# Optimization experiments

Measured on AMD Instinct MI355X. Metric: run time of the kernel, lower is better.

The kernel has to match this reference:

```python
import jax, jax.numpy as jnp
import numpy as np

B, D = 500000, 3
EPS = 1e-8

def _matrix_sqrt_H(A):
    # Hermitian sqrt via eigh: Q diag((L^2)^0.25) Q^T  (matches torch code incl. |L| handling)
    L, Q = jnp.linalg.eigh(A)
    return jnp.einsum('bij,bj,bkj->bik', Q, (L ** 2) ** 0.25, Q)

def setup_inputs() -> dict:
    key = jax.random.key(0)
    k1, k2, k3, k4 = jax.random.split(key, 4)
    miu_1 = jax.random.normal(k1, (B, D), dtype=jnp.float32)
    miu_2 = jax.random.normal(k2, (B, D), dtype=jnp.float32)
    eye = jnp.eye(D, dtype=jnp.float32)
    M1 = jax.random.normal(k3, (B, D, D), dtype=jnp.float32)
    M2 = jax.random.normal(k4, (B, D, D), dtype=jnp.float32)
    # SPD covariances, as produced by a Gaussian-splatting pipeline
    cov_1 = 0.1 * jnp.einsum('bij,bkj->bik', M1, M1) + 1e-3 * eye
    cov_2 = 0.1 * jnp.einsum('bij,bkj->bik', M2, M2) + 1e-3 * eye
    return {"miu_1": miu_1, "miu_2": miu_2, "cov_1": cov_1, "cov_2": cov_2}

def reference(miu_1, miu_2, cov_1, cov_2):
    eye = jnp.eye(cov_1.shape[-1], dtype=cov_1.dtype)
    A_sqrt = _matrix_sqrt_H(cov_1 + eye * EPS)
    A_sqrt_inv = jnp.linalg.inv(A_sqrt + eye * EPS)
    C = jnp.einsum('bij,bjk,blk->bil', A_sqrt, cov_2, A_sqrt)  # A_sqrt cov_2 A_sqrt^T
    C_sqrt = _matrix_sqrt_H(C + eye * EPS)
    cov_velocity = jnp.einsum('bij,bjk,blk->bil', A_sqrt, C_sqrt, A_sqrt_inv)
    cov_velocity = cov_velocity + jnp.swapaxes(cov_velocity, -1, -2) - 2.0 * cov_1
    return (miu_2 - miu_1, cov_velocity)
```

## Files before the change

kernel.cpp:

```cpp
#include <hip/hip_runtime.h>
#include <math.h>

#define EPS 1e-8f

typedef float f4a __attribute__((ext_vector_type(4), aligned(4)));
typedef float f2a __attribute__((ext_vector_type(2), aligned(4)));

static __device__ __forceinline__ void jangle(float app, float aqq, float apq,
                                              float &c, float &s, float &app2, float &aqq2) {
    float h     = aqq - app;
    float ah    = fabsf(h) + 1e-18f;
    float v     = apq + apq;
    float rad   = fmaf(ah, ah, v * v);
    float rr    = __builtin_amdgcn_rsqf(rad);
    float c2h   = fmaf(0.5f * ah, rr, 0.5f);
    float rc2   = __builtin_amdgcn_rsqf(c2h);
    c = c2h * rc2;
    float apq_s = (h < 0.0f) ? -apq : apq;
    s = apq_s * (rr * rc2);
    float dl    = copysignf(0.5f * (rad * rr - ah), h);
    app2 = app - dl;
    aqq2 = aqq + dl;
}

static __device__ __forceinline__ void eigh3(
    float &a00, float &a01, float &a02, float &a11, float &a12, float &a22,
    float &q00, float &q01, float &q02,
    float &q10, float &q11, float &q12,
    float &q20, float &q21, float &q22)
{
    float c, s, x, y, t0, t1;
    jangle(a00, a11, a01, c, s, x, y); a00 = x; a11 = y; a01 = 0.0f;
    t0 = a02; t1 = a12; a02 = fmaf(c, t0, -s * t1); a12 = fmaf(c, t1, s * t0);
    q00 = c; q01 = s; q10 = -s; q11 = c;

    jangle(a00, a22, a02, c, s, x, y); a00 = x; a22 = y; a02 = 0.0f;
    t0 = a01; t1 = a12; a01 = fmaf(c, t0, -s * t1); a12 = fmaf(c, t1, s * t0);
    q02 = s * q00; q12 = s * q10; q20 = -s; q22 = c;
    q00 = c * q00; q10 = c * q10;

    jangle(a11, a22, a12, c, s, x, y); a11 = x; a22 = y; a12 = 0.0f;
    t0 = a01; t1 = a02; a01 = fmaf(c, t0, -s * t1); a02 = fmaf(c, t1, s * t0);
    t0 = q01; t1 = q02; q01 = fmaf(c, t0, -s * t1); q02 = fmaf(s, t0, c * t1);
    t0 = q11; t1 = q12; q11 = fmaf(c, t0, -s * t1); q12 = fmaf(s, t0, c * t1);
    q21 = -s * q22; q22 = c * q22;

    #pragma unroll
    for (int sw = 0; sw < 2; ++sw) {
        jangle(a00, a11, a01, c, s, x, y); a00 = x; a11 = y; a01 = 0.0f;
        t0 = a02; t1 = a12; a02 = fmaf(c, t0, -s * t1); a12 = fmaf(c, t1, s * t0);
        t0 = q00; t1 = q01; q00 = fmaf(c, t0, -s * t1); q01 = fmaf(s, t0, c * t1);
        t0 = q10; t1 = q11; q10 = fmaf(c, t0, -s * t1); q11 = fmaf(s, t0, c * t1);
        t0 = q20; t1 = q21; q20 = fmaf(c, t0, -s * t1); q21 = fmaf(s, t0, c * t1);

        jangle(a00, a22, a02, c, s, x, y); a00 = x; a22 = y; a02 = 0.0f;
        t0 = a01; t1 = a12; a01 = fmaf(c, t0, -s * t1); a12 = fmaf(c, t1, s * t0);
        t0 = q00; t1 = q02; q00 = fmaf(c, t0, -s * t1); q02 = fmaf(s, t0, c * t1);
        t0 = q10; t1 = q12; q10 = fmaf(c, t0, -s * t1); q12 = fmaf(s, t0, c * t1);
        t0 = q20; t1 = q22; q20 = fmaf(c, t0, -s * t1); q22 = fmaf(s, t0, c * t1);

        jangle(a11, a22, a12, c, s, x, y); a11 = x; a22 = y; a12 = 0.0f;
        t0 = a01; t1 = a02; a01 = fmaf(c, t0, -s * t1); a02 = fmaf(c, t1, s * t0);
        t0 = q01; t1 = q02; q01 = fmaf(c, t0, -s * t1); q02 = fmaf(s, t0, c * t1);
        t0 = q11; t1 = q12; q11 = fmaf(c, t0, -s * t1); q12 = fmaf(s, t0, c * t1);
        t0 = q21; t1 = q22; q21 = fmaf(c, t0, -s * t1); q22 = fmaf(s, t0, c * t1);
    }
}

static __device__ __forceinline__ void wlog_elem(
    float k00, float k01, float k02, float k11, float k12, float k22,
    float m00, float m01, float m02, float m11, float m12, float m22,
    float &o00, float &o01, float &o02, float &o11, float &o12, float &o22)
{
    float a00 = k00 + EPS, a01 = k01, a02 = k02,
          a11 = k11 + EPS, a12 = k12, a22 = k22 + EPS;
    float q00, q01, q02, q10, q11, q12, q20, q21, q22;
    eigh3(a00, a01, a02, a11, a12, a22,
          q00, q01, q02, q10, q11, q12, q20, q21, q22);

    float w0 = fmaxf(fabsf(a00), 1e-12f);
    float w1 = fmaxf(fabsf(a11), 1e-12f);
    float w2 = fmaxf(fabsf(a22), 1e-12f);
    float di0 = __builtin_amdgcn_rsqf(w0), di1 = __builtin_amdgcn_rsqf(w1),
          di2 = __builtin_amdgcn_rsqf(w2);
    float d0 = w0 * di0, d1 = w1 * di1, d2 = w2 * di2;

    float T00 = fmaf(m00, q00, fmaf(m01, q10, m02 * q20));
    float T01 = fmaf(m00, q01, fmaf(m01, q11, m02 * q21));
    float T02 = fmaf(m00, q02, fmaf(m01, q12, m02 * q22));
    float T10 = fmaf(m01, q00, fmaf(m11, q10, m12 * q20));
    float T11 = fmaf(m01, q01, fmaf(m11, q11, m12 * q21));
    float T12 = fmaf(m01, q02, fmaf(m11, q12, m12 * q22));
    float T20 = fmaf(m02, q00, fmaf(m12, q10, m22 * q20));
    float T21 = fmaf(m02, q01, fmaf(m12, q11, m22 * q21));
    float T22 = fmaf(m02, q02, fmaf(m12, q12, m22 * q22));

    float g00 = fmaf(q00, T00, fmaf(q10, T10, q20 * T20));
    float g01 = fmaf(q00, T01, fmaf(q10, T11, q20 * T21));
    float g02 = fmaf(q00, T02, fmaf(q10, T12, q20 * T22));
    float g11 = fmaf(q01, T01, fmaf(q11, T11, q21 * T21));
    float g12 = fmaf(q01, T02, fmaf(q11, T12, q21 * T22));
    float g22 = fmaf(q02, T02, fmaf(q12, T12, q22 * T22));

    float cp00 = fmaf(w0, g00, EPS);
    float cp11 = fmaf(w1, g11, EPS);
    float cp22 = fmaf(w2, g22, EPS);
    float cp01 = d0 * d1 * g01;
    float cp02 = d0 * d2 * g02;
    float cp12 = d1 * d2 * g12;

    float e00, e01, e02, e10, e11, e12, e20, e21, e22;
    eigh3(cp00, cp01, cp02, cp11, cp12, cp22,
          e00, e01, e02, e10, e11, e12, e20, e21, e22);
    float u0 = fmaxf(fabsf(cp00), 1e-12f);
    float u1 = fmaxf(fabsf(cp11), 1e-12f);
    float u2 = fmaxf(fabsf(cp22), 1e-12f);
    float ts0 = u0 * __builtin_amdgcn_rsqf(u0);
    float ts1 = u1 * __builtin_amdgcn_rsqf(u1);
    float ts2 = u2 * __builtin_amdgcn_rsqf(u2);

    float Ed00 = d0*e00, Ed01 = d0*e01, Ed02 = d0*e02;
    float Ed10 = d1*e10, Ed11 = d1*e11, Ed12 = d1*e12;
    float Ed20 = d2*e20, Ed21 = d2*e21, Ed22 = d2*e22;
    float Ei00 = di0*e00, Ei01 = di0*e01, Ei02 = di0*e02;
    float Ei10 = di1*e10, Ei11 = di1*e11, Ei12 = di1*e12;
    float Ei20 = di2*e20, Ei21 = di2*e21, Ei22 = di2*e22;

    float U00 = fmaf(q00, Ed00, fmaf(q01, Ed10, q02 * Ed20));
    float U01 = fmaf(q00, Ed01, fmaf(q01, Ed11, q02 * Ed21));
    float U02 = fmaf(q00, Ed02, fmaf(q01, Ed12, q02 * Ed22));
    float U10 = fmaf(q10, Ed00, fmaf(q11, Ed10, q12 * Ed20));
    float U11 = fmaf(q10, Ed01, fmaf(q11, Ed11, q12 * Ed21));
    float U12 = fmaf(q10, Ed02, fmaf(q11, Ed12, q12 * Ed22));
    float U20 = fmaf(q20, Ed00, fmaf(q21, Ed10, q22 * Ed20));
    float U21 = fmaf(q20, Ed01, fmaf(q21, Ed11, q22 * Ed21));
    float U22 = fmaf(q20, Ed02, fmaf(q21, Ed12, q22 * Ed22));

    float P00 = fmaf(q00, Ei00, fmaf(q01, Ei10, q02 * Ei20));
    float P01 = fmaf(q00, Ei01, fmaf(q01, Ei11, q02 * Ei21));
    float P02 = fmaf(q00, Ei02, fmaf(q01, Ei12, q02 * Ei22));
    float P10 = fmaf(q10, Ei00, fmaf(q11, Ei10, q12 * Ei20));
    float P11 = fmaf(q10, Ei01, fmaf(q11, Ei11, q12 * Ei21));
    float P12 = fmaf(q10, Ei02, fmaf(q11, Ei12, q12 * Ei22));
    float P20 = fmaf(q20, Ei00, fmaf(q21, Ei10, q22 * Ei20));
    float P21 = fmaf(q20, Ei01, fmaf(q21, Ei11, q22 * Ei21));
    float P22 = fmaf(q20, Ei02, fmaf(q21, Ei12, q22 * Ei22));

    float A0 = ts0 * U00, A1 = ts1 * U01, A2 = ts2 * U02;
    float B0 = ts0 * U10, B1 = ts1 * U11, B2 = ts2 * U12;
    float C0 = ts0 * U20, C1 = ts1 * U21, C2 = ts2 * U22;

    float W00 = 2.0f * fmaf(A0, P00, fmaf(A1, P01, A2 * P02));
    float W11 = 2.0f * fmaf(B0, P10, fmaf(B1, P11, B2 * P12));
    float W22 = 2.0f * fmaf(C0, P20, fmaf(C1, P21, C2 * P22));
    float W01 = fmaf(A0, P10, fmaf(A1, P11, fmaf(A2, P12,
                fmaf(B0, P00, fmaf(B1, P01, B2 * P02)))));
    float W02 = fmaf(A0, P20, fmaf(A1, P21, fmaf(A2, P22,
                fmaf(C0, P00, fmaf(C1, P01, C2 * P02)))));
    float W12 = fmaf(B0, P20, fmaf(B1, P21, fmaf(B2, P22,
                fmaf(C0, P10, fmaf(C1, P11, C2 * P12)))));

    o00 = fmaf(-2.0f, k00, W00);
    o01 = fmaf(-2.0f, k01, W01);
    o02 = fmaf(-2.0f, k02, W02);
    o11 = fmaf(-2.0f, k11, W11);
    o12 = fmaf(-2.0f, k12, W12);
    o22 = fmaf(-2.0f, k22, W22);
}

__global__ __launch_bounds__(256) void wasserstein_log_kernel(
    const float* __restrict__ miu1, const float* __restrict__ miu2,
    const float* __restrict__ cov1, const float* __restrict__ cov2,
    float* __restrict__ out, int B)
{
    int b0 = blockIdx.x * blockDim.x + threadIdx.x;
    int nT = (B + 1) >> 1;
    if (b0 >= nT) return;

    if (2 * b0 + 1 < B) {
        size_t cb = 18 * (size_t)b0;
        const f4a* p1 = (const f4a*)(cov1 + cb);
        f4a Pa0 = p1[0], Pa1 = p1[1], Pa2 = p1[2], Pa3 = p1[3];
        f2a Pa4 = *(const f2a*)(cov1 + cb + 16);
        const f4a* p2 = (const f4a*)(cov2 + cb);
        f4a Pb0 = p2[0], Pb1 = p2[1], Pb2 = p2[2], Pb3 = p2[3];
        f2a Pb4 = *(const f2a*)(cov2 + cb + 16);

        size_t mb = 6 * (size_t)b0;
        f4a M10 = *(const f4a*)(miu1 + mb);
        f2a M11 = *(const f2a*)(miu1 + mb + 4);
        f4a M20 = *(const f4a*)(miu2 + mb);
        f2a M21 = *(const f2a*)(miu2 + mb + 4);

        f4a UM; UM.x = M20.x - M10.x; UM.y = M20.y - M10.y;
                UM.z = M20.z - M10.z; UM.w = M20.w - M10.w;
        f2a UM2; UM2.x = M21.x - M11.x; UM2.y = M21.y - M11.y;
        *(f4a*)(out + mb) = UM;
        *(f2a*)(out + mb + 4) = UM2;

        float oA00, oA01, oA02, oA11, oA12, oA22;
        wlog_elem(Pa0.x, Pa0.y, Pa0.z, Pa1.x, Pa1.y, Pa2.x,
                  Pb0.x, Pb0.y, Pb0.z, Pb1.x, Pb1.y, Pb2.x,
                  oA00, oA01, oA02, oA11, oA12, oA22);
        float oB00, oB01, oB02, oB11, oB12, oB22;
        wlog_elem(Pa2.y, Pa2.z, Pa2.w, Pa3.y, Pa3.z, Pa4.y,
                  Pb2.y, Pb2.z, Pb2.w, Pb3.y, Pb3.z, Pb4.y,
                  oB00, oB01, oB02, oB11, oB12, oB22);

        float* oc = out + 3 * (size_t)B + cb;
        f4a S0; S0.x = oA00; S0.y = oA01; S0.z = oA02; S0.w = oA01;
        f4a S1; S1.x = oA11; S1.y = oA12; S1.z = oA02; S1.w = oA12;
        f4a S2; S2.x = oA22; S2.y = oB00; S2.z = oB01; S2.w = oB02;
        f4a S3; S3.x = oB01; S3.y = oB11; S3.z = oB12; S3.w = oB02;
        f2a S4; S4.x = oB12; S4.y = oB22;
        ((f4a*)oc)[0] = S0; ((f4a*)oc)[1] = S1;
        ((f4a*)oc)[2] = S2; ((f4a*)oc)[3] = S3;
        *(f2a*)(oc + 16) = S4;
    } else {
        int b = B - 1;
        size_t cb = 9 * (size_t)b;
        float k00 = cov1[cb+0], k01 = cov1[cb+1], k02 = cov1[cb+2],
              k11 = cov1[cb+4], k12 = cov1[cb+5], k22 = cov1[cb+8];
        float m00 = cov2[cb+0], m01 = cov2[cb+1], m02 = cov2[cb+2],
              m11 = cov2[cb+4], m12 = cov2[cb+5], m22 = cov2[cb+8];
        size_t mbs = 3 * (size_t)b;
        out[mbs+0] = miu2[mbs+0] - miu1[mbs+0];
        out[mbs+1] = miu2[mbs+1] - miu1[mbs+1];
        out[mbs+2] = miu2[mbs+2] - miu1[mbs+2];
        float o00, o01, o02, o11, o12, o22;
        wlog_elem(k00, k01, k02, k11, k12, k22,
                  m00, m01, m02, m11, m12, m22,
                  o00, o01, o02, o11, o12, o22);
        float* oc = out + 3 * (size_t)B + cb;
        oc[0] = o00; oc[1] = o01; oc[2] = o02;
        oc[3] = o01; oc[4] = o11; oc[5] = o12;
        oc[6] = o02; oc[7] = o12; oc[8] = o22;
    }
}

extern "C" void kernel_launch(void* const* d_in, const int* in_sizes, int n_in,
                              void* d_out, int out_size, void* d_ws, size_t ws_size,
                              hipStream_t stream) {
    const float* miu1 = (const float*)d_in[0];
    const float* miu2 = (const float*)d_in[1];
    const float* cov1 = (const float*)d_in[2];
    const float* cov2 = (const float*)d_in[3];
    float* out = (float*)d_out;
    int B  = in_sizes[0] / 3;
    int nT = (B + 1) / 2;
    int threads = 256;
    int blocks = (nT + threads - 1) / threads;
    hipLaunchKernelGGL(wasserstein_log_kernel, dim3(blocks), dim3(threads), 0, stream,
                       miu1, miu2, cov1, cov2, out, B);
}
```

Before: 99.61 us.

## Replace two Jacobi eigendecompositions with closed-form sqrt of cov1·cov2 via invariants

Drops both per-element 3x3 Jacobi eigen solves. The new code forms P = cov1·cov2, takes its invariants, and solves a quartic by Newton iteration to get the trace of sqrt(P). It then builds sqrt(P) = (t·P + d·I)(P + mI)^-1 with a cofactor inverse, using the identity A^½ (A^½ B A^½)^½ A^-½ = (AB)^½. This cuts the ALU and transcendental work per element, at the cost of possible precision loss for ill-conditioned matrices and dependence on the fixed Newton iteration count.

```diff
diff --git a/kernel.cpp b/kernel.cpp
--- a/kernel.cpp
+++ b/kernel.cpp
@@ -6,166 +6,85 @@
 typedef float f4a __attribute__((ext_vector_type(4), aligned(4)));
 typedef float f2a __attribute__((ext_vector_type(2), aligned(4)));
 
-static __device__ __forceinline__ void jangle(float app, float aqq, float apq,
-                                              float &c, float &s, float &app2, float &aqq2) {
-    float h     = aqq - app;
-    float ah    = fabsf(h) + 1e-18f;
-    float v     = apq + apq;
-    float rad   = fmaf(ah, ah, v * v);
-    float rr    = __builtin_amdgcn_rsqf(rad);
-    float c2h   = fmaf(0.5f * ah, rr, 0.5f);
-    float rc2   = __builtin_amdgcn_rsqf(c2h);
-    c = c2h * rc2;
-    float apq_s = (h < 0.0f) ? -apq : apq;
-    s = apq_s * (rr * rc2);
-    float dl    = copysignf(0.5f * (rad * rr - ah), h);
-    app2 = app - dl;
-    aqq2 = aqq + dl;
-}
-
-static __device__ __forceinline__ void eigh3(
-    float &a00, float &a01, float &a02, float &a11, float &a12, float &a22,
-    float &q00, float &q01, float &q02,
-    float &q10, float &q11, float &q12,
-    float &q20, float &q21, float &q22)
-{
-    float c, s, x, y, t0, t1;
-    jangle(a00, a11, a01, c, s, x, y); a00 = x; a11 = y; a01 = 0.0f;
-    t0 = a02; t1 = a12; a02 = fmaf(c, t0, -s * t1); a12 = fmaf(c, t1, s * t0);
-    q00 = c; q01 = s; q10 = -s; q11 = c;
-
-    jangle(a00, a22, a02, c, s, x, y); a00 = x; a22 = y; a02 = 0.0f;
-    t0 = a01; t1 = a12; a01 = fmaf(c, t0, -s * t1); a12 = fmaf(c, t1, s * t0);
-    q02 = s * q00; q12 = s * q10; q20 = -s; q22 = c;
-    q00 = c * q00; q10 = c * q10;
-
-    jangle(a11, a22, a12, c, s, x, y); a11 = x; a22 = y; a12 = 0.0f;
-    t0 = a01; t1 = a02; a01 = fmaf(c, t0, -s * t1); a02 = fmaf(c, t1, s * t0);
-    t0 = q01; t1 = q02; q01 = fmaf(c, t0, -s * t1); q02 = fmaf(s, t0, c * t1);
-    t0 = q11; t1 = q12; q11 = fmaf(c, t0, -s * t1); q12 = fmaf(s, t0, c * t1);
-    q21 = -s * q22; q22 = c * q22;
-
-    #pragma unroll
-    for (int sw = 0; sw < 2; ++sw) {
-        jangle(a00, a11, a01, c, s, x, y); a00 = x; a11 = y; a01 = 0.0f;
-        t0 = a02; t1 = a12; a02 = fmaf(c, t0, -s * t1); a12 = fmaf(c, t1, s * t0);
-        t0 = q00; t1 = q01; q00 = fmaf(c, t0, -s * t1); q01 = fmaf(s, t0, c * t1);
-        t0 = q10; t1 = q11; q10 = fmaf(c, t0, -s * t1); q11 = fmaf(s, t0, c * t1);
-        t0 = q20; t1 = q21; q20 = fmaf(c, t0, -s * t1); q21 = fmaf(s, t0, c * t1);
-
-        jangle(a00, a22, a02, c, s, x, y); a00 = x; a22 = y; a02 = 0.0f;
-        t0 = a01; t1 = a12; a01 = fmaf(c, t0, -s * t1); a12 = fmaf(c, t1, s * t0);
-        t0 = q00; t1 = q02; q00 = fmaf(c, t0, -s * t1); q02 = fmaf(s, t0, c * t1);
-        t0 = q10; t1 = q12; q10 = fmaf(c, t0, -s * t1); q12 = fmaf(s, t0, c * t1);
-        t0 = q20; t1 = q22; q20 = fmaf(c, t0, -s * t1); q22 = fmaf(s, t0, c * t1);
-
-        jangle(a11, a22, a12, c, s, x, y); a11 = x; a22 = y; a12 = 0.0f;
-        t0 = a01; t1 = a02; a01 = fmaf(c, t0, -s * t1); a02 = fmaf(c, t1, s * t0);
-        t0 = q01; t1 = q02; q01 = fmaf(c, t0, -s * t1); q02 = fmaf(s, t0, c * t1);
-        t0 = q11; t1 = q12; q11 = fmaf(c, t0, -s * t1); q12 = fmaf(s, t0, c * t1);
-        t0 = q21; t1 = q22; q21 = fmaf(c, t0, -s * t1); q22 = fmaf(s, t0, c * t1);
-    }
-}
-
 static __device__ __forceinline__ void wlog_elem(
     float k00, float k01, float k02, float k11, float k12, float k22,
     float m00, float m01, float m02, float m11, float m12, float m22,
     float &o00, float &o01, float &o02, float &o11, float &o12, float &o22)
 {
-    float a00 = k00 + EPS, a01 = k01, a02 = k02,
-          a11 = k11 + EPS, a12 = k12, a22 = k22 + EPS;
-    float q00, q01, q02, q10, q11, q12, q20, q21, q22;
-    eigh3(a00, a01, a02, a11, a12, a22,
-          q00, q01, q02, q10, q11, q12, q20, q21, q22);
+    float e00 = k00 + EPS, e11 = k11 + EPS, e22 = k22 + EPS;
 
-    float w0 = fmaxf(fabsf(a00), 1e-12f);
-    float w1 = fmaxf(fabsf(a11), 1e-12f);
-    float w2 = fmaxf(fabsf(a22), 1e-12f);
-    float di0 = __builtin_amdgcn_rsqf(w0), di1 = __builtin_amdgcn_rsqf(w1),
-          di2 = __builtin_amdgcn_rsqf(w2);
-    float d0 = w0 * di0, d1 = w1 * di1, d2 = w2 * di2;
+    float P00 = fmaf(e00, m00, fmaf(k01, m01, k02 * m02));
+    float P01 = fmaf(e00, m01, fmaf(k01, m11, k02 * m12));
+    float P02 = fmaf(e00, m02, fmaf(k01, m12, k02 * m22));
+    float P10 = fmaf(k01, m00, fmaf(e11, m01, k12 * m02));
+    float P11 = fmaf(k01, m01, fmaf(e11, m11, k12 * m12));
+    float P12 = fmaf(k01, m02, fmaf(e11, m12, k12 * m22));
+    float P20 = fmaf(k02, m00, fmaf(k12, m01, e22 * m02));
+    float P21 = fmaf(k02, m01, fmaf(k12, m11, e22 * m12));
+    float P22 = fmaf(k02, m02, fmaf(k12, m12, e22 * m22));
 
-    float T00 = fmaf(m00, q00, fmaf(m01, q10, m02 * q20));
-    float T01 = fmaf(m00, q01, fmaf(m01, q11, m02 * q21));
-    float T02 = fmaf(m00, q02, fmaf(m01, q12, m02 * q22));
-    float T10 = fmaf(m01, q00, fmaf(m11, q10, m12 * q20));
-    float T11 = fmaf(m01, q01, fmaf(m11, q11, m12 * q21));
-    float T12 = fmaf(m01, q02, fmaf(m11, q12, m12 * q22));
-    float T20 = fmaf(m02, q00, fmaf(m12, q10, m22 * q20));
-    float T21 = fmaf(m02, q01, fmaf(m12, q11, m22 * q21));
-    float T22 = fmaf(m02, q02, fmaf(m12, q12, m22 * q22));
+    float I1 = P00 + P11 + P22;
+    float I2 = fmaf(P00, P11, -P01 * P10)
+             + fmaf(P00, P22, -P02 * P20)
+             + fmaf(P11, P22, -P12 * P21);
+    float dK = fmaf(e00, fmaf(e11, e22, -k12 * k12),
+               fmaf(-k01, fmaf(k01, e22, -k12 * k02),
+                     k02 * fmaf(k01, k12, -e11 * k02)));
+    float dM = fmaf(m00, fmaf(m11, m22, -m12 * m12),
+               fmaf(-m01, fmaf(m01, m22, -m12 * m02),
+                     m02 * fmaf(m01, m12, -m11 * m02)));
+    float I3 = fmaxf(dK * dM, 1e-30f);
+    float d  = sqrtf(I3);
 
-    float g00 = fmaf(q00, T00, fmaf(q10, T10, q20 * T20));
-    float g01 = fmaf(q00, T01, fmaf(q10, T11, q20 * T21));
-    float g02 = fmaf(q00, T02, fmaf(q10, T12, q20 * T22));
-    float g11 = fmaf(q01, T01, fmaf(q11, T11, q21 * T21));
-    float g12 = fmaf(q01, T02, fmaf(q11, T12, q21 * T22));
-    float g22 = fmaf(q02, T02, fmaf(q12, T12, q22 * T22));
+    float I1p  = fmaxf(I1, 1e-30f);
+    float m_up = sqrtf(fmaxf(fmaf(2.0f * sqrtf(3.0f * I1p), d, I2), 0.0f));
+    float t    = sqrtf(fmaf(2.0f, m_up, I1p));
+    float K2   = fmaf(I1, I1, -4.0f * I2);
+    float I1_2 = I1 + I1;
+    float I1_4 = I1_2 + I1_2;
+    float d8   = 8.0f * d;
+    #pragma unroll
+    for (int it = 0; it < 5; ++it) {
+        float t2 = t * t;
+        float f  = fmaf(t2, t2 - I1_2, fmaf(-d8, t, K2));
+        float fp = fmaf(t, fmaf(4.0f, t2, -I1_4), -d8);
+        t = fmaf(-f, __builtin_amdgcn_rcpf(fp), t);
+    }
+    float m = 0.5f * fmaf(t, t, -I1);
 
-    float cp00 = fmaf(w0, g00, EPS);
-    float cp11 = fmaf(w1, g11, EPS);
-    float cp22 = fmaf(w2, g22, EPS);
-    float cp01 = d0 * d1 * g01;
-    float cp02 = d0 * d2 * g02;
-    float cp12 = d1 * d2 * g12;
+    float N00 = P00 + m, N11 = P11 + m, N22 = P22 + m;
+    float C00 = fmaf(N11, N22, -P12 * P21);
+    float C01 = fmaf(P12, P20, -P10 * N22);
+    float C02 = fmaf(P10, P21, -N11 * P20);
+    float C10 = fmaf(P02, P21, -P01 * N22);
+    float C11 = fmaf(N00, N22, -P02 * P20);
+    float C12 = fmaf(P01, P20, -N00 * P21);
+    float C20 = fmaf(P01, P12, -P02 * N11);
+    float C21 = fmaf(P02, P10, -N00 * P12);
+    float C22 = fmaf(N00, N11, -P01 * P10);
+    float det = fmaf(N00, C00, fmaf(P01, C01, P02 * C02));
+    float rdet = __builtin_amdgcn_rcpf(det);
 
-    float e00, e01, e02, e10, e11, e12, e20, e21, e22;
-    eigh3(cp00, cp01, cp02, cp11, cp12, cp22,
-          e00, e01, e02, e10, e11, e12, e20, e21, e22);
-    float u0 = fmaxf(fabsf(cp00), 1e-12f);
-    float u1 = fmaxf(fabsf(cp11), 1e-12f);
-    float u2 = fmaxf(fabsf(cp22), 1e-12f);
-    float ts0 = u0 * __builtin_amdgcn_rsqf(u0);
-    float ts1 = u1 * __builtin_amdgcn_rsqf(u1);
-    float ts2 = u2 * __builtin_amdgcn_rsqf(u2);
+    float Y00 = fmaf(t, P00, d), Y01 = t * P01, Y02 = t * P02;
+    float Y10 = t * P10, Y11 = fmaf(t, P11, d), Y12 = t * P12;
+    float Y20 = t * P20, Y21 = t * P21, Y22 = fmaf(t, P22, d);
 
-    float Ed00 = d0*e00, Ed01 = d0*e01, Ed02 = d0*e02;
-    float Ed10 = d1*e10, Ed11 = d1*e11, Ed12 = d1*e12;
-    float Ed20 = d2*e20, Ed21 = d2*e21, Ed22 = d2*e22;
-    float Ei00 = di0*e00, Ei01 = di0*e01, Ei02 = di0*e02;
-    float Ei10 = di1*e10, Ei11 = di1*e11, Ei12 = di1*e12;
-    float Ei20 = di2*e20, Ei21 = di2*e21, Ei22 = di2*e22;
+    float Z00 = fmaf(Y00, C00, fmaf(Y01, C01, Y02 * C02));
+    float Z01 = fmaf(Y00, C10, fmaf(Y01, C11, Y02 * C12));
+    float Z02 = fmaf(Y00, C20, fmaf(Y01, C21, Y02 * C22));
+    float Z10 = fmaf(Y10, C00, fmaf(Y11, C01, Y12 * C02));
+    float Z11 = fmaf(Y10, C10, fmaf(Y11, C11, Y12 * C12));
+    float Z12 = fmaf(Y10, C20, fmaf(Y11, C21, Y12 * C22));
+    float Z20 = fmaf(Y20, C00, fmaf(Y21, C01, Y22 * C02));
+    float Z21 = fmaf(Y20, C10, fmaf(Y21, C11, Y22 * C12));
+    float Z22 = fmaf(Y20, C20, fmaf(Y21, C21, Y22 * C22));
 
-    float U00 = fmaf(q00, Ed00, fmaf(q01, Ed10, q02 * Ed20));
-    float U01 = fmaf(q00, Ed01, fmaf(q01, Ed11, q02 * Ed21));
-    float U02 = fmaf(q00, Ed02, fmaf(q01, Ed12, q02 * Ed22));
-    float U10 = fmaf(q10, Ed00, fmaf(q11, Ed10, q12 * Ed20));
-    float U11 = fmaf(q10, Ed01, fmaf(q11, Ed11, q12 * Ed21));
-    float U12 = fmaf(q10, Ed02, fmaf(q11, Ed12, q12 * Ed22));
-    float U20 = fmaf(q20, Ed00, fmaf(q21, Ed10, q22 * Ed20));
-    float U21 = fmaf(q20, Ed01, fmaf(q21, Ed11, q22 * Ed21));
-    float U22 = fmaf(q20, Ed02, fmaf(q21, Ed12, q22 * Ed22));
-
-    float P00 = fmaf(q00, Ei00, fmaf(q01, Ei10, q02 * Ei20));
-    float P01 = fmaf(q00, Ei01, fmaf(q01, Ei11, q02 * Ei21));
-    float P02 = fmaf(q00, Ei02, fmaf(q01, Ei12, q02 * Ei22));
-    float P10 = fmaf(q10, Ei00, fmaf(q11, Ei10, q12 * Ei20));
-    float P11 = fmaf(q10, Ei01, fmaf(q11, Ei11, q12 * Ei21));
-    float P12 = fmaf(q10, Ei02, fmaf(q11, Ei12, q12 * Ei22));
-    float P20 = fmaf(q20, Ei00, fmaf(q21, Ei10, q22 * Ei20));
-    float P21 = fmaf(q20, Ei01, fmaf(q21, Ei11, q22 * Ei21));
-    float P22 = fmaf(q20, Ei02, fmaf(q21, Ei12, q22 * Ei22));
-
-    float A0 = ts0 * U00, A1 = ts1 * U01, A2 = ts2 * U02;
-    float B0 = ts0 * U10, B1 = ts1 * U11, B2 = ts2 * U12;
-    float C0 = ts0 * U20, C1 = ts1 * U21, C2 = ts2 * U22;
-
-    float W00 = 2.0f * fmaf(A0, P00, fmaf(A1, P01, A2 * P02));
-    float W11 = 2.0f * fmaf(B0, P10, fmaf(B1, P11, B2 * P12));
-    float W22 = 2.0f * fmaf(C0, P20, fmaf(C1, P21, C2 * P22));
-    float W01 = fmaf(A0, P10, fmaf(A1, P11, fmaf(A2, P12,
-                fmaf(B0, P00, fmaf(B1, P01, B2 * P02)))));
-    float W02 = fmaf(A0, P20, fmaf(A1, P21, fmaf(A2, P22,
-                fmaf(C0, P00, fmaf(C1, P01, C2 * P02)))));
-    float W12 = fmaf(B0, P20, fmaf(B1, P21, fmaf(B2, P22,
-                fmaf(C0, P10, fmaf(C1, P11, C2 * P12)))));
-
-    o00 = fmaf(-2.0f, k00, W00);
-    o01 = fmaf(-2.0f, k01, W01);
-    o02 = fmaf(-2.0f, k02, W02);
-    o11 = fmaf(-2.0f, k11, W11);
-    o12 = fmaf(-2.0f, k12, W12);
-    o22 = fmaf(-2.0f, k22, W22);
+    o00 = fmaf(rdet, Z00 + Z00, -2.0f * k00);
+    o01 = fmaf(rdet, Z01 + Z10, -2.0f * k01);
+    o02 = fmaf(rdet, Z02 + Z20, -2.0f * k02);
+    o11 = fmaf(rdet, Z11 + Z11, -2.0f * k11);
+    o12 = fmaf(rdet, Z12 + Z21, -2.0f * k12);
+    o22 = fmaf(rdet, Z22 + Z22, -2.0f * k22);
 }
 
 __global__ __launch_bounds__(256) void wasserstein_log_kernel(
```

Result: no change. 99.19 us (-0.4%).
